# Performance work log

Hardware: AMD Instinct MI355X
Metric: run time of the kernel (lower is better)

The kernel has to match this reference:

```python
import jax, jax.numpy as jnp
import numpy as np

SEQ_LEN, BATCH = 1024, 256
VOCAB, EMBED, HIDDEN = 32000, 512, 1024


def setup_inputs() -> dict:
    key = jax.random.key(0)
    k1, k2, k3, k4, k5, k6 = jax.random.split(key, 6)
    return {
        "x_seq": jax.random.randint(k1, (SEQ_LEN, BATCH), 0, VOCAB, dtype=jnp.int64)
        if jax.config.jax_enable_x64 else jax.random.randint(k1, (SEQ_LEN, BATCH), 0, VOCAB, dtype=jnp.int32),
        "emb": jax.random.normal(k2, (VOCAB, EMBED), dtype=jnp.float32) * 0.02,
        "W_ih": jax.random.normal(k3, (HIDDEN, EMBED), dtype=jnp.float32) * 0.02,
        "b_ih": jax.random.normal(k4, (HIDDEN,), dtype=jnp.float32) * 0.02,
        "W_hh": jax.random.normal(k5, (HIDDEN, HIDDEN), dtype=jnp.float32) * 0.02,
        "b_hh": jax.random.normal(k6, (HIDDEN,), dtype=jnp.float32) * 0.02,
    }


def reference(x_seq, emb, W_ih, b_ih, W_hh, b_hh):
    # x_seq: [S, B] int -> embedded: [S, B, E]
    embedded = emb[x_seq]
    # Input projection is time-independent: batch it into one big GEMM
    # (same math as per-step W_ih(x_t) + bias in the torch loop).
    x_proj = jnp.einsum("sbe,he->sbh", embedded, W_ih) + b_ih  # [S, B, H]

    h0 = jnp.zeros((x_seq.shape[1], W_hh.shape[0]), dtype=emb.dtype)

    def step(h, xp_t):
        # h_{t} = tanh(W_ih x_t + b_ih + W_hh h_{t-1} + b_hh)
        h_new = jnp.tanh(xp_t + h @ W_hh.T + b_hh)
        return h_new, h_new

    _, hidden_states = jax.lax.scan(step, h0, x_proj)  # [S, B, H]
    return hidden_states
```

## Files before the change

### kernel.cpp

```cpp
#include <hip/hip_runtime.h>
#include <hip/hip_bf16.h>

typedef unsigned short u16;
typedef unsigned int u32;
typedef unsigned long long u64;
typedef __attribute__((ext_vector_type(8))) short short8v;
typedef __attribute__((ext_vector_type(8))) unsigned short ushort8v;
typedef __attribute__((ext_vector_type(4))) float float4v;
typedef __attribute__((ext_vector_type(4))) unsigned int uint4v;
typedef __attribute__((ext_vector_type(2))) unsigned int uint2v;

#define S_LEN 1024
#define BATCH 256
#define VOCAB 32000
#define EMBED 512
#define HIDDEN 1024
#define BH (BATCH * HIDDEN)
#define FLAG_STRIDE 32

__device__ inline u16 f2bf(float f) {
  return __builtin_bit_cast(u16, __float2bfloat16(f));
}

__device__ inline short8v cohload16(const u16* base, int voff) {
  __amdgpu_buffer_rsrc_t r =
      __builtin_amdgcn_make_buffer_rsrc((void*)base, (short)0, -1, 0x00020000);
  uint4v d = __builtin_amdgcn_raw_buffer_load_b128(r, voff, 0, 17);
  return __builtin_bit_cast(short8v, d);
}
__device__ inline void cohstore8(u16* base, int voff, uint2v v) {
  __amdgpu_buffer_rsrc_t r =
      __builtin_amdgcn_make_buffer_rsrc((void*)base, (short)0, -1, 0x00020000);
  __builtin_amdgcn_raw_buffer_store_b64(v, r, voff, 0, 17);
}

__device__ inline short8v cvt8(float4v a, float4v b) {
  ushort8v v;
  v[0]=f2bf(a[0]); v[1]=f2bf(a[1]); v[2]=f2bf(a[2]); v[3]=f2bf(a[3]);
  v[4]=f2bf(b[0]); v[5]=f2bf(b[1]); v[6]=f2bf(b[2]); v[7]=f2bf(b[3]);
  return __builtin_bit_cast(short8v, v);
}

__global__ __launch_bounds__(256) void prep_kernel(u16* __restrict__ ws16) {
  int i = blockIdx.x * 256 + threadIdx.x;
  ushort8v z = {0,0,0,0,0,0,0,0};
  *(ushort8v*)(ws16 + (size_t)i * 8) = z;
}

__global__ __launch_bounds__(256, 1) void rnn_fused(const int* __restrict__ xseq,
                                                    const float* __restrict__ emb,
                                                    const float* __restrict__ wih,
                                                    const float* __restrict__ bih,
                                                    const float* __restrict__ whh,
                                                    const float* __restrict__ bhh,
                                                    u16* __restrict__ hbuf,
                                                    float* __restrict__ out,
                                                    u32* __restrict__ flag) {
  __shared__ float red[4][16][68];
  __shared__ u16 xq[S_LEN * 16];
  const int tid = threadIdx.x;
  const int lane = tid & 63, w = tid >> 6;
  const int l15 = lane & 15, l4 = lane >> 4;
  const int g = blockIdx.x & 15;
  const int jt = blockIdx.x >> 4;

  short8v Wf[4][8];
  #pragma unroll
  for (int jj = 0; jj < 4; jj++)
    #pragma unroll
    for (int kq = 0; kq < 8; kq++) {
      const float* s = whh + (size_t)(jt * 64 + jj * 16 + l15) * HIDDEN
                       + w * 256 + kq * 32 + l4 * 8;
      Wf[jj][kq] = cvt8(*(const float4v*)s, *(const float4v*)(s + 4));
    }
  short8v Wihf[4][4];
  #pragma unroll
  for (int jj = 0; jj < 4; jj++)
    #pragma unroll
    for (int kk = 0; kk < 4; kk++) {
      const float* s = wih + (size_t)(jt * 64 + jj * 16 + l15) * EMBED
                       + w * 128 + kk * 32 + l4 * 8;
      Wihf[jj][kk] = cvt8(*(const float4v*)s, *(const float4v*)(s + 4));
    }
  for (int i = tid; i < S_LEN * 16; i += 256)
    xq[i] = (u16)xseq[(i >> 4) * BATCH + g * 16 + (i & 15)];
  const int trow = w * 4 + (lane >> 4);
  const int tc4 = (lane & 15) * 4;
  float bsum[4];
  #pragma unroll
  for (int i = 0; i < 4; i++)
    bsum[i] = bhh[jt * 64 + tc4 + i] + bih[jt * 64 + tc4 + i];
  const int aoff = ((g * 16 + l15) * HIDDEN + w * 256 + l4 * 8) * 2;
  const int hoff = ((g * 16 + trow) * HIDDEN + jt * 64 + tc4) * 2;
  __syncthreads();

  float4v xacc[4] = {};
  {
    const float* er = emb + (size_t)xq[l15] * EMBED + w * 128 + l4 * 8;
    #pragma unroll
    for (int kk = 0; kk < 4; kk++) {
      short8v af = cvt8(*(const float4v*)(er + kk * 32),
                        *(const float4v*)(er + kk * 32 + 4));
      #pragma unroll
      for (int jj = 0; jj < 4; jj++)
        xacc[jj] = __builtin_amdgcn_mfma_f32_16x16x32_bf16(af, Wihf[jj][kk], xacc[jj], 0, 0, 0);
    }
  }

  for (int t = 0; t < S_LEN; t++) {
    const int p = t & 1;
    float* outt = out + (size_t)t * BH;
    float4v accp[4] = {xacc[0], xacc[1], xacc[2], xacc[3]};
    if (t > 0) {
      if (lane < 16) {
        const u32* f = flag + ((size_t)(g * 16 + w * 4 + (lane >> 2)) * 4 + (lane & 3)) * FLAG_STRIDE;
        while (__hip_atomic_load(f, __ATOMIC_RELAXED, __HIP_MEMORY_SCOPE_AGENT) < (u32)t) { }
      }
    }
    __builtin_amdgcn_sched_barrier(0);
    const u16* hp = hbuf + (size_t)p * BH;
    short8v a[8];
    #pragma unroll
    for (int kq = 0; kq < 8; kq++)
      a[kq] = cohload16(hp, aoff + kq * 64);
    __builtin_amdgcn_sched_barrier(0);
    int tn = (t + 1 < S_LEN) ? (t + 1) : t;
    const float* er = emb + (size_t)xq[tn * 16 + l15] * EMBED + w * 128 + l4 * 8;
    float4v e[8];
    #pragma unroll
    for (int kk = 0; kk < 4; kk++) {
      e[2 * kk]     = *(const float4v*)(er + kk * 32);
      e[2 * kk + 1] = *(const float4v*)(er + kk * 32 + 4);
    }
    #pragma unroll
    for (int kq = 0; kq < 8; kq++)
      #pragma unroll
      for (int jj = 0; jj < 4; jj++)
        accp[jj] = __builtin_amdgcn_mfma_f32_16x16x32_bf16(a[kq], Wf[jj][kq], accp[jj], 0, 0, 0);
    #pragma unroll
    for (int jj = 0; jj < 4; jj++)
      #pragma unroll
      for (int q = 0; q < 4; q++)
        red[w][l4 * 4 + q][jj * 16 + l15] = accp[jj][q];
    __syncthreads();
    float4v r0 = *(const float4v*)&red[0][trow][tc4];
    float4v r1 = *(const float4v*)&red[1][trow][tc4];
    float4v r2 = *(const float4v*)&red[2][trow][tc4];
    float4v r3 = *(const float4v*)&red[3][trow][tc4];
    __syncthreads();
    float th[4];
    #pragma unroll
    for (int i = 0; i < 4; i++) {
      float s = r0[i] + r1[i] + r2[i] + r3[i] + bsum[i];
      float ex = __expf(-2.0f * fabsf(s));
      float v = (1.0f - ex) / (1.0f + ex);
      th[i] = copysignf(v, s);
    }
    float4v o = {th[0], th[1], th[2], th[3]};
    *(float4v*)(outt + (size_t)(g * 16 + trow) * HIDDEN + jt * 64 + tc4) = o;
    uint2v hv;
    hv[0] = (u32)f2bf(th[0]) | ((u32)f2bf(th[1]) << 16);
    hv[1] = (u32)f2bf(th[2]) | ((u32)f2bf(th[3]) << 16);
    u16* hq = hbuf + (size_t)(p ^ 1) * BH;
    cohstore8(hq, hoff, hv);
    asm volatile("s_waitcnt vmcnt(0)" ::: "memory");
    if (lane == 0)
      __hip_atomic_store(flag + ((size_t)(g * 16 + jt) * 4 + w) * FLAG_STRIDE,
                         (u32)(t + 1), __ATOMIC_RELAXED, __HIP_MEMORY_SCOPE_AGENT);
    float4v xn[4] = {};
    #pragma unroll
    for (int kk = 0; kk < 4; kk++) {
      short8v af = cvt8(e[2 * kk], e[2 * kk + 1]);
      #pragma unroll
      for (int jj = 0; jj < 4; jj++)
        xn[jj] = __builtin_amdgcn_mfma_f32_16x16x32_bf16(af, Wihf[jj][kk], xn[jj], 0, 0, 0);
    }
    xacc[0] = xn[0]; xacc[1] = xn[1]; xacc[2] = xn[2]; xacc[3] = xn[3];
  }
}

extern "C" void kernel_launch(void* const* d_in, const int* in_sizes, int n_in,
                              void* d_out, int out_size, void* d_ws, size_t ws_size,
                              hipStream_t stream) {
  const int* xseq   = (const int*)d_in[0];
  const float* emb  = (const float*)d_in[1];
  const float* wih  = (const float*)d_in[2];
  const float* bih  = (const float*)d_in[3];
  const float* whh  = (const float*)d_in[4];
  const float* bhh  = (const float*)d_in[5];
  float* out = (float*)d_out;
  char* ws = (char*)d_ws;
  u16* hbuf = (u16*)ws;
  u32* flag = (u32*)(ws + 1048576);

  prep_kernel<<<288, 256, 0, stream>>>((u16*)ws);
  rnn_fused<<<256, 256, 0, stream>>>(xseq, emb, wih, bih, whh, bhh, hbuf, out, flag);
}
```

Before: 3.342 ms.

## Pre-convert embeddings to bf16, double-buffer reduction smem, defer output store

The prep kernel now also converts the full fp32 embedding table to bf16 in workspace when space allows, so the recurrent loop gathers half the bytes and skips per-step conversion. The shared reduction buffer is double-buffered by step parity, which removes the second __syncthreads per timestep. The fp32 output store is moved after the flag publish so the next step's dependents are signalled sooner. The cost is an extra full-table conversion pass (about 65 MB read) before the loop, and a larger dynamic shared-memory allocation.

```diff
diff --git a/kernel.cpp b/kernel.cpp
--- a/kernel.cpp
+++ b/kernel.cpp
@@ -3,7 +3,6 @@
 
 typedef unsigned short u16;
 typedef unsigned int u32;
-typedef unsigned long long u64;
 typedef __attribute__((ext_vector_type(8))) short short8v;
 typedef __attribute__((ext_vector_type(8))) unsigned short ushort8v;
 typedef __attribute__((ext_vector_type(4))) float float4v;
@@ -41,10 +40,23 @@
   return __builtin_bit_cast(short8v, v);
 }
 
-__global__ __launch_bounds__(256) void prep_kernel(u16* __restrict__ ws16) {
+__global__ __launch_bounds__(256) void prep_kernel(u16* __restrict__ ws16,
+                                                   const float* __restrict__ emb,
+                                                   u16* __restrict__ emb16,
+                                                   int do_emb) {
   int i = blockIdx.x * 256 + threadIdx.x;
-  ushort8v z = {0,0,0,0,0,0,0,0};
-  *(ushort8v*)(ws16 + (size_t)i * 8) = z;
+  const int NZ = 73728;
+  if (i < NZ) {
+    ushort8v z = {0,0,0,0,0,0,0,0};
+    *(ushort8v*)(ws16 + (size_t)i * 8) = z;
+  } else if (do_emb) {
+    int j = i - NZ;
+    if (j < (VOCAB * EMBED) / 8) {
+      const float* s = emb + (size_t)j * 8;
+      *(ushort8v*)(emb16 + (size_t)j * 8) = __builtin_bit_cast(
+          ushort8v, cvt8(*(const float4v*)s, *(const float4v*)(s + 4)));
+    }
+  }
 }
 
 __global__ __launch_bounds__(256, 1) void rnn_fused(const int* __restrict__ xseq,
@@ -55,9 +67,12 @@
                                                     const float* __restrict__ bhh,
                                                     u16* __restrict__ hbuf,
                                                     float* __restrict__ out,
-                                                    u32* __restrict__ flag) {
-  __shared__ float red[4][16][68];
-  __shared__ u16 xq[S_LEN * 16];
+                                                    u32* __restrict__ flag,
+                                                    const u16* __restrict__ emb16,
+                                                    int eb16) {
+  extern __shared__ u16 smem[];
+  u16* xq = smem;
+  float (*red)[4][16][68] = (float (*)[4][16][68])(smem + S_LEN * 16);
   const int tid = threadIdx.x;
   const int lane = tid & 63, w = tid >> 6;
   const int l15 = lane & 15, l4 = lane >> 4;
@@ -95,12 +110,21 @@
   __syncthreads();
 
   float4v xacc[4] = {};
-  {
-    const float* er = emb + (size_t)xq[l15] * EMBED + w * 128 + l4 * 8;
-    #pragma unroll
-    for (int kk = 0; kk < 4; kk++) {
-      short8v af = cvt8(*(const float4v*)(er + kk * 32),
-                        *(const float4v*)(er + kk * 32 + 4));
+  if (eb16) {
+    const u16* er0 = emb16 + (size_t)xq[l15] * EMBED + w * 128 + l4 * 8;
+    #pragma unroll
+    for (int kk = 0; kk < 4; kk++) {
+      short8v af = *(const short8v*)(er0 + kk * 32);
+      #pragma unroll
+      for (int jj = 0; jj < 4; jj++)
+        xacc[jj] = __builtin_amdgcn_mfma_f32_16x16x32_bf16(af, Wihf[jj][kk], xacc[jj], 0, 0, 0);
+    }
+  } else {
+    const float* er0 = emb + (size_t)xq[l15] * EMBED + w * 128 + l4 * 8;
+    #pragma unroll
+    for (int kk = 0; kk < 4; kk++) {
+      short8v af = cvt8(*(const float4v*)(er0 + kk * 32),
+                        *(const float4v*)(er0 + kk * 32 + 4));
       #pragma unroll
       for (int jj = 0; jj < 4; jj++)
         xacc[jj] = __builtin_amdgcn_mfma_f32_16x16x32_bf16(af, Wihf[jj][kk], xacc[jj], 0, 0, 0);
@@ -113,7 +137,8 @@
     float4v accp[4] = {xacc[0], xacc[1], xacc[2], xacc[3]};
     if (t > 0) {
       if (lane < 16) {
-        const u32* f = flag + ((size_t)(g * 16 + w * 4 + (lane >> 2)) * 4 + (lane & 3)) * FLAG_STRIDE;
+        const u32* f = flag +
+            ((size_t)(g * 16 + w * 4 + (lane >> 2)) * 4 + (lane & 3)) * FLAG_STRIDE;
         while (__hip_atomic_load(f, __ATOMIC_RELAXED, __HIP_MEMORY_SCOPE_AGENT) < (u32)t) { }
       }
     }
@@ -125,12 +150,20 @@
       a[kq] = cohload16(hp, aoff + kq * 64);
     __builtin_amdgcn_sched_barrier(0);
     int tn = (t + 1 < S_LEN) ? (t + 1) : t;
-    const float* er = emb + (size_t)xq[tn * 16 + l15] * EMBED + w * 128 + l4 * 8;
+    short8v ebf[4];
     float4v e[8];
-    #pragma unroll
-    for (int kk = 0; kk < 4; kk++) {
-      e[2 * kk]     = *(const float4v*)(er + kk * 32);
-      e[2 * kk + 1] = *(const float4v*)(er + kk * 32 + 4);
+    if (eb16) {
+      const u16* er = emb16 + (size_t)xq[tn * 16 + l15] * EMBED + w * 128 + l4 * 8;
+      #pragma unroll
+      for (int kk = 0; kk < 4; kk++)
+        ebf[kk] = *(const short8v*)(er + kk * 32);
+    } else {
+      const float* er = emb + (size_t)xq[tn * 16 + l15] * EMBED + w * 128 + l4 * 8;
+      #pragma unroll
+      for (int kk = 0; kk < 4; kk++) {
+        e[2 * kk]     = *(const float4v*)(er + kk * 32);
+        e[2 * kk + 1] = *(const float4v*)(er + kk * 32 + 4);
+      }
     }
     #pragma unroll
     for (int kq = 0; kq < 8; kq++)
@@ -141,13 +174,12 @@
     for (int jj = 0; jj < 4; jj++)
       #pragma unroll
       for (int q = 0; q < 4; q++)
-        red[w][l4 * 4 + q][jj * 16 + l15] = accp[jj][q];
+        red[p][w][l4 * 4 + q][jj * 16 + l15] = accp[jj][q];
     __syncthreads();
-    float4v r0 = *(const float4v*)&red[0][trow][tc4];
-    float4v r1 = *(const float4v*)&red[1][trow][tc4];
-    float4v r2 = *(const float4v*)&red[2][trow][tc4];
-    float4v r3 = *(const float4v*)&red[3][trow][tc4];
-    __syncthreads();
+    float4v r0 = *(const float4v*)&red[p][0][trow][tc4];
+    float4v r1 = *(const float4v*)&red[p][1][trow][tc4];
+    float4v r2 = *(const float4v*)&red[p][2][trow][tc4];
+    float4v r3 = *(const float4v*)&red[p][3][trow][tc4];
     float th[4];
     #pragma unroll
     for (int i = 0; i < 4; i++) {
@@ -156,8 +188,6 @@
       float v = (1.0f - ex) / (1.0f + ex);
       th[i] = copysignf(v, s);
     }
-    float4v o = {th[0], th[1], th[2], th[3]};
-    *(float4v*)(outt + (size_t)(g * 16 + trow) * HIDDEN + jt * 64 + tc4) = o;
     uint2v hv;
     hv[0] = (u32)f2bf(th[0]) | ((u32)f2bf(th[1]) << 16);
     hv[1] = (u32)f2bf(th[2]) | ((u32)f2bf(th[3]) << 16);
@@ -167,10 +197,12 @@
     if (lane == 0)
       __hip_atomic_store(flag + ((size_t)(g * 16 + jt) * 4 + w) * FLAG_STRIDE,
                          (u32)(t + 1), __ATOMIC_RELAXED, __HIP_MEMORY_SCOPE_AGENT);
+    float4v o = {th[0], th[1], th[2], th[3]};
+    *(float4v*)(outt + (size_t)(g * 16 + trow) * HIDDEN + jt * 64 + tc4) = o;
     float4v xn[4] = {};
     #pragma unroll
     for (int kk = 0; kk < 4; kk++) {
-      short8v af = cvt8(e[2 * kk], e[2 * kk + 1]);
+      short8v af = eb16 ? ebf[kk] : cvt8(e[2 * kk], e[2 * kk + 1]);
       #pragma unroll
       for (int jj = 0; jj < 4; jj++)
         xn[jj] = __builtin_amdgcn_mfma_f32_16x16x32_bf16(af, Wihf[jj][kk], xn[jj], 0, 0, 0);
@@ -190,9 +222,17 @@
   const float* bhh  = (const float*)d_in[5];
   float* out = (float*)d_out;
   char* ws = (char*)d_ws;
-  u16* hbuf = (u16*)ws;
-  u32* flag = (u32*)(ws + 1048576);
-
-  prep_kernel<<<288, 256, 0, stream>>>((u16*)ws);
-  rnn_fused<<<256, 256, 0, stream>>>(xseq, emb, wih, bih, whh, bhh, hbuf, out, flag);
-}
+  u16* hbuf  = (u16*)ws;
+  u32* flag  = (u32*)(ws + 1048576);
+  u16* emb16 = (u16*)(ws + 1179648);
+
+  const size_t need = 1179648u + (size_t)VOCAB * EMBED * 2u;
+  const int do_emb = (ws_size >= need) ? 1 : 0;
+  const int prep_items = 73728 + (do_emb ? (VOCAB * EMBED) / 8 : 0);
+
+  prep_kernel<<<(prep_items + 255) / 256, 256, 0, stream>>>((u16*)ws, emb, emb16, do_emb);
+  (void)hipFuncSetAttribute((const void*)rnn_fused,
+                            hipFuncAttributeMaxDynamicSharedMemorySize, 67584);
+  rnn_fused<<<256, 256, 67584, stream>>>(xseq, emb, wih, bih, whh, bhh,
+                                         hbuf, out, flag, emb16, do_emb);
+}
```

After: 3.359 ms. Within noise of the previous version (+0.5%).
